# Kernel optimization log

Hardware: AMD Instinct MI355X
Metric: run time of the kernel (lower is better)

Reference implementation:

```python
import jax, jax.numpy as jnp
import numpy as np

NUM_HEADS = 8
EPS = 1e-3

N_TOKENS = 32768
DIM = 256
N_WIN = 128
WIN = N_TOKENS // N_WIN  # 256 tokens per window


def setup_inputs() -> dict:
    key = jax.random.key(0)
    ks = jax.random.split(key, 4)
    x = jax.random.normal(ks[0], (N_TOKENS, DIM), dtype=jnp.float32)
    # torch nn.Linear weights are [out_features, in_features]
    w_qkv = jax.random.normal(ks[1], (3 * DIM, DIM), dtype=jnp.float32) * (DIM ** -0.5)
    w_proj = jax.random.normal(ks[2], (DIM, DIM), dtype=jnp.float32) * (DIM ** -0.5)
    b_proj = jnp.zeros((DIM,), dtype=jnp.float32)
    batch_win_inds = (jnp.arange(N_TOKENS) // WIN).astype(jnp.int64)
    offsets = (jnp.arange(N_WIN) * WIN).astype(jnp.int64)
    counts = jnp.full((N_WIN,), WIN, dtype=jnp.int64)
    return {"x": x, "w_qkv": w_qkv, "w_proj": w_proj, "b_proj": b_proj,
            "offsets": offsets, "counts": counts, "batch_win_inds": batch_win_inds}


def reference(x, w_qkv, w_proj, b_proj, offsets, counts, batch_win_inds):
    N, C = x.shape
    H = NUM_HEADS
    hd = C // H
    W = counts.shape[0]  # number of windows (static)

    qkv = x @ w_qkv.T                      # [N, 3C]
    q, k, v = jnp.split(qkv, 3, axis=-1)   # each [N, C]
    q = jax.nn.relu(q.reshape(N, H, hd))   # [N, H, hd]
    k = jax.nn.relu(k.reshape(N, H, hd))
    v = v.reshape(N, H, hd)

    seg = batch_win_inds.astype(jnp.int32)
    # per-window KV state: kv[w] = sum_{i in w} k_i^T v_i   -> [W, H, hd, hd]
    kv = jax.ops.segment_sum(jnp.einsum('nhc,nhd->nhcd', k, v), seg, num_segments=W)
    # per-window key sum for normalizer                      -> [W, H, hd]
    s = jax.ops.segment_sum(k, seg, num_segments=W)

    y = jnp.einsum('nhc,nhcd->nhd', q, kv[seg])              # [N, H, hd]
    z = jnp.sum(s[seg] * q, axis=-1, keepdims=True)          # [N, H, 1]
    y = y / (z + EPS)

    y = y.reshape(N, C) @ w_proj.T + b_proj                  # [N, C]
    return y
```

## Files before the change

kernel.cpp:

```cpp
#include <hip/hip_runtime.h>

typedef __bf16 bf16_t;
typedef bf16_t bf16x8 __attribute__((ext_vector_type(8)));
typedef bf16_t bf16x4 __attribute__((ext_vector_type(4)));
typedef float f32x4 __attribute__((ext_vector_type(4)));

#define KDIM 256
#define NWIN 128
#define WIN  256

__device__ __forceinline__ bf16x8 cvt8(f32x4 a, f32x4 b) {
    bf16x8 o;
    o[0] = (bf16_t)a[0]; o[1] = (bf16_t)a[1]; o[2] = (bf16_t)a[2]; o[3] = (bf16_t)a[3];
    o[4] = (bf16_t)b[0]; o[5] = (bf16_t)b[1]; o[6] = (bf16_t)b[2]; o[7] = (bf16_t)b[3];
    return o;
}

template<int A_FP32, int F32OUT>
__global__ __launch_bounds__(256) void gemm_lds(
    const void* __restrict__ A_,
    const float* __restrict__ Bw,
    void* __restrict__ Cout,
    int N,
    const float* __restrict__ bias,
    int relu_cols)
{
    __shared__ __align__(16) bf16_t As[128 * 40];
    __shared__ __align__(16) bf16_t Bs[128 * 40];

    const int tid  = threadIdx.x;
    const int lane = tid & 63;
    const int wv   = tid >> 6;
    const int wm   = wv >> 1;
    const int wn   = wv & 1;
    const int m0   = blockIdx.x * 128;
    const int n0   = blockIdx.y * 128;
    const int r    = lane & 15;
    const int q    = lane >> 4;
    const int srow = tid >> 1;
    const int shalf = tid & 1;

    f32x4 acc[4][4] = {};

#pragma unroll
    for (int kc = 0; kc < KDIM; kc += 32) {
        if (A_FP32) {
            const float* ap = (const float*)A_ + (size_t)(m0 + srow) * KDIM + kc + shalf * 16;
            f32x4 f0 = *(const f32x4*)(ap + 0);
            f32x4 f1 = *(const f32x4*)(ap + 4);
            f32x4 f2 = *(const f32x4*)(ap + 8);
            f32x4 f3 = *(const f32x4*)(ap + 12);
            *(bf16x8*)(&As[srow * 40 + shalf * 16 + 0]) = cvt8(f0, f1);
            *(bf16x8*)(&As[srow * 40 + shalf * 16 + 8]) = cvt8(f2, f3);
        } else {
            const bf16_t* ap = (const bf16_t*)A_ + (size_t)(m0 + srow) * KDIM + kc + shalf * 16;
            bf16x8 h0 = *(const bf16x8*)(ap + 0);
            bf16x8 h1 = *(const bf16x8*)(ap + 8);
            *(bf16x8*)(&As[srow * 40 + shalf * 16 + 0]) = h0;
            *(bf16x8*)(&As[srow * 40 + shalf * 16 + 8]) = h1;
        }
        {
            const float* bp = Bw + (size_t)(n0 + srow) * KDIM + kc + shalf * 16;
            f32x4 f0 = *(const f32x4*)(bp + 0);
            f32x4 f1 = *(const f32x4*)(bp + 4);
            f32x4 f2 = *(const f32x4*)(bp + 8);
            f32x4 f3 = *(const f32x4*)(bp + 12);
            *(bf16x8*)(&Bs[srow * 40 + shalf * 16 + 0]) = cvt8(f0, f1);
            *(bf16x8*)(&Bs[srow * 40 + shalf * 16 + 8]) = cvt8(f2, f3);
        }
        __syncthreads();

        bf16x8 a[4], b[4];
#pragma unroll
        for (int i = 0; i < 4; ++i)
            a[i] = *(const bf16x8*)(&As[(wm * 64 + i * 16 + r) * 40 + q * 8]);
#pragma unroll
        for (int j = 0; j < 4; ++j)
            b[j] = *(const bf16x8*)(&Bs[(wn * 64 + j * 16 + r) * 40 + q * 8]);
#pragma unroll
        for (int i = 0; i < 4; ++i)
#pragma unroll
            for (int j = 0; j < 4; ++j)
                acc[i][j] = __builtin_amdgcn_mfma_f32_16x16x32_bf16(a[i], b[j], acc[i][j], 0, 0, 0);
        __syncthreads();
    }

#pragma unroll
    for (int i = 0; i < 4; ++i) {
#pragma unroll
        for (int j = 0; j < 4; ++j) {
            const int colg = n0 + wn * 64 + j * 16 + r;
            float badd = bias ? bias[colg] : 0.0f;
#pragma unroll
            for (int reg = 0; reg < 4; ++reg) {
                const int rowg = m0 + wm * 64 + i * 16 + q * 4 + reg;
                float v = acc[i][j][reg] + badd;
                if (colg < relu_cols) v = fmaxf(v, 0.0f);
                const size_t idx = (size_t)rowg * N + colg;
                if (F32OUT) ((float*)Cout)[idx] = v;
                else        ((bf16_t*)Cout)[idx] = (bf16_t)v;
            }
        }
    }
}

__global__ __launch_bounds__(256) void kvy_kernel(
    const bf16_t* __restrict__ QKV,
    const int* __restrict__ offsets,
    const int* __restrict__ counts,
    bf16_t* __restrict__ Y)
{
    const int w = blockIdx.x;
    const int h = blockIdx.y;
    const int is64 = (counts[1] == 0) ? 1 : 0;
    const int off = offsets[w << is64];
    const int tid = threadIdx.x;
    const int lane = tid & 63;
    const int wv = tid >> 6;

    __shared__ __align__(16) bf16_t KT[32 * 264];
    __shared__ __align__(16) bf16_t VT[32 * 264];
    __shared__ __align__(16) bf16_t KVT[32 * 40];
    __shared__ float sbuf[32];
    __shared__ float spart[32 * 8];
    __shared__ float zinv[WIN];

    {
        const int t = tid;
        const bf16_t* kp = QKV + (size_t)(off + t) * 768 + 256 + h * 32;
        const bf16_t* vp = kp + 256;
        bf16_t ka[32], va[32];
#pragma unroll
        for (int u = 0; u < 4; ++u) {
            bf16x8 kk = *(const bf16x8*)(kp + u * 8);
            bf16x8 vvv = *(const bf16x8*)(vp + u * 8);
#pragma unroll
            for (int j = 0; j < 8; ++j) { ka[u * 8 + j] = kk[j]; va[u * 8 + j] = vvv[j]; }
        }
#pragma unroll
        for (int c = 0; c < 32; ++c) {
            KT[c * 264 + t] = ka[c];
            VT[c * 264 + t] = va[c];
        }
    }
    __syncthreads();

    {
        const int c = tid >> 3;
        const int tc = (tid & 7) * 32;
        float ps = 0.f;
#pragma unroll
        for (int u = 0; u < 4; ++u) {
            bf16x8 kk = *(const bf16x8*)(&KT[c * 264 + tc + u * 8]);
#pragma unroll
            for (int j = 0; j < 8; ++j) ps += (float)kk[j];
        }
        spart[c * 8 + (tid & 7)] = ps;
    }
    {
        const int i = wv >> 1, j = wv & 1;
        const int r = lane & 15, q = lane >> 4;
        f32x4 acc = {};
#pragma unroll
        for (int ch = 0; ch < 8; ++ch) {
            bf16x8 af = *(const bf16x8*)(&KT[(i * 16 + r) * 264 + ch * 32 + q * 8]);
            bf16x8 bf_ = *(const bf16x8*)(&VT[(j * 16 + r) * 264 + ch * 32 + q * 8]);
            acc = __builtin_amdgcn_mfma_f32_16x16x32_bf16(af, bf_, acc, 0, 0, 0);
        }
        bf16x4 kv4;
#pragma unroll
        for (int reg = 0; reg < 4; ++reg) kv4[reg] = (bf16_t)acc[reg];
        *(bf16x4*)(&KVT[(j * 16 + r) * 40 + i * 16 + q * 4]) = kv4;
    }
    __syncthreads();
    if (tid < 32) {
        float s = 0.f;
#pragma unroll
        for (int u = 0; u < 8; ++u) s += spart[tid * 8 + u];
        sbuf[tid] = s;
    }
    __syncthreads();

    {
        const int t = tid;
        const bf16_t* qp = QKV + (size_t)(off + t) * 768 + h * 32;
        float z = 0.f;
#pragma unroll
        for (int u = 0; u < 4; ++u) {
            bf16x8 qq = *(const bf16x8*)(qp + u * 8);
#pragma unroll
            for (int j = 0; j < 8; ++j) z += (float)qq[j] * sbuf[u * 8 + j];
        }
        zinv[t] = 1.0f / (z + 1e-3f);
    }
    __syncthreads();

    {
        const int r = lane & 15, q = lane >> 4;
        bf16x8 b0 = *(const bf16x8*)(&KVT[(r) * 40 + q * 8]);
        bf16x8 b1 = *(const bf16x8*)(&KVT[(16 + r) * 40 + q * 8]);
#pragma unroll
        for (int u = 0; u < 4; ++u) {
            const int mi = wv * 4 + u;
            const bf16_t* ap = QKV + (size_t)(off + mi * 16 + r) * 768 + h * 32 + q * 8;
            bf16x8 af = *(const bf16x8*)ap;
            f32x4 acc0 = {}, acc1 = {};
            acc0 = __builtin_amdgcn_mfma_f32_16x16x32_bf16(af, b0, acc0, 0, 0, 0);
            acc1 = __builtin_amdgcn_mfma_f32_16x16x32_bf16(af, b1, acc1, 0, 0, 0);
#pragma unroll
            for (int reg = 0; reg < 4; ++reg) {
                const int row = mi * 16 + q * 4 + reg;
                const float zi = zinv[row];
                bf16_t* yp = Y + (size_t)(off + row) * 256 + h * 32;
                yp[r]      = (bf16_t)(acc0[reg] * zi);
                yp[16 + r] = (bf16_t)(acc1[reg] * zi);
            }
        }
    }
}

extern "C" void kernel_launch(void* const* d_in, const int* in_sizes, int n_in,
                              void* d_out, int out_size, void* d_ws, size_t ws_size,
                              hipStream_t stream) {
    const float* x      = (const float*)d_in[0];
    const float* w_qkv  = (const float*)d_in[1];
    const float* w_proj = (const float*)d_in[2];
    const float* b_proj = (const float*)d_in[3];
    const int*   offs   = (const int*)d_in[4];
    const int*   cnts   = (const int*)d_in[5];

    const int NX = in_sizes[0];
    const int M  = NX / KDIM;

    char* ws = (char*)d_ws;
    bf16_t* QKV = (bf16_t*)ws;
    bf16_t* Y   = (bf16_t*)(ws + 50331648);
    float*  out = (float*)d_out;

    gemm_lds<1, 0><<<dim3(M / 128, 768 / 128), 256, 0, stream>>>(
        (const void*)x, w_qkv, (void*)QKV, 768, nullptr, 512);

    kvy_kernel<<<dim3(NWIN, 8), 256, 0, stream>>>(QKV, offs, cnts, Y);

    gemm_lds<0, 1><<<dim3(M / 128, 256 / 128), 256, 0, stream>>>(
        (const void*)Y, w_proj, (void*)out, 256, b_proj, 0);
}
```

Baseline: 156.8 us.

## Stage full K=256 tiles in LDS once and drop per-chunk barriers in GEMMs

The GEMM kernels now load the entire 128x256 A and B tiles into dynamic LDS (about 132 KB) in one up-front phase, then run all eight k-chunks of MFMA with no __syncthreads in the loop. This removes 16 barriers per block and lets the global loads issue back-to-back instead of one small chunk at a time. The cost is a large LDS footprint that allows only one block per CU, and no overlap between loading and compute, since the whole load phase finishes before any MFMA work starts.

```diff
diff --git a/kernel.cpp b/kernel.cpp
--- a/kernel.cpp
+++ b/kernel.cpp
@@ -8,6 +8,8 @@
 #define KDIM 256
 #define NWIN 128
 #define WIN  256
+#define LDS_STRIDE 264
+#define GEMM_LDS_BYTES (2 * 128 * LDS_STRIDE * 2)
 
 __device__ __forceinline__ bf16x8 cvt8(f32x4 a, f32x4 b) {
     bf16x8 o;
@@ -17,7 +19,7 @@
 }
 
 template<int A_FP32, int F32OUT>
-__global__ __launch_bounds__(256) void gemm_lds(
+__global__ __launch_bounds__(256) void gemm_os(
     const void* __restrict__ A_,
     const float* __restrict__ Bw,
     void* __restrict__ Cout,
@@ -25,64 +27,62 @@
     const float* __restrict__ bias,
     int relu_cols)
 {
-    __shared__ __align__(16) bf16_t As[128 * 40];
-    __shared__ __align__(16) bf16_t Bs[128 * 40];
-
-    const int tid  = threadIdx.x;
+    extern __shared__ __align__(16) bf16_t lds[];
+    bf16_t* As = lds;
+    bf16_t* Bs = lds + 128 * LDS_STRIDE;
+
+    const int tid = threadIdx.x;
+    const int m0 = blockIdx.x * 128;
+    const int n0 = blockIdx.y * 128;
+
+    const int srow = tid >> 1;
+    const int sh   = (tid & 1) * 128;
+
+    if (A_FP32) {
+        const float* ap = (const float*)A_ + (size_t)(m0 + srow) * KDIM + sh;
+#pragma unroll
+        for (int u = 0; u < 16; ++u) {
+            f32x4 f0 = *(const f32x4*)(ap + u * 8);
+            f32x4 f1 = *(const f32x4*)(ap + u * 8 + 4);
+            *(bf16x8*)(&As[srow * LDS_STRIDE + sh + u * 8]) = cvt8(f0, f1);
+        }
+    } else {
+        const bf16_t* ap = (const bf16_t*)A_ + (size_t)(m0 + srow) * KDIM + sh;
+#pragma unroll
+        for (int u = 0; u < 16; ++u)
+            *(bf16x8*)(&As[srow * LDS_STRIDE + sh + u * 8]) = *(const bf16x8*)(ap + u * 8);
+    }
+    {
+        const float* bp = Bw + (size_t)(n0 + srow) * KDIM + sh;
+#pragma unroll
+        for (int u = 0; u < 16; ++u) {
+            f32x4 f0 = *(const f32x4*)(bp + u * 8);
+            f32x4 f1 = *(const f32x4*)(bp + u * 8 + 4);
+            *(bf16x8*)(&Bs[srow * LDS_STRIDE + sh + u * 8]) = cvt8(f0, f1);
+        }
+    }
+    __syncthreads();
+
     const int lane = tid & 63;
-    const int wv   = tid >> 6;
-    const int wm   = wv >> 1;
-    const int wn   = wv & 1;
-    const int m0   = blockIdx.x * 128;
-    const int n0   = blockIdx.y * 128;
-    const int r    = lane & 15;
-    const int q    = lane >> 4;
-    const int srow = tid >> 1;
-    const int shalf = tid & 1;
+    const int wv = tid >> 6;
+    const int wm = wv >> 1, wn = wv & 1;
+    const int r = lane & 15, q = lane >> 4;
 
     f32x4 acc[4][4] = {};
-
 #pragma unroll
     for (int kc = 0; kc < KDIM; kc += 32) {
-        if (A_FP32) {
-            const float* ap = (const float*)A_ + (size_t)(m0 + srow) * KDIM + kc + shalf * 16;
-            f32x4 f0 = *(const f32x4*)(ap + 0);
-            f32x4 f1 = *(const f32x4*)(ap + 4);
-            f32x4 f2 = *(const f32x4*)(ap + 8);
-            f32x4 f3 = *(const f32x4*)(ap + 12);
-            *(bf16x8*)(&As[srow * 40 + shalf * 16 + 0]) = cvt8(f0, f1);
-            *(bf16x8*)(&As[srow * 40 + shalf * 16 + 8]) = cvt8(f2, f3);
-        } else {
-            const bf16_t* ap = (const bf16_t*)A_ + (size_t)(m0 + srow) * KDIM + kc + shalf * 16;
-            bf16x8 h0 = *(const bf16x8*)(ap + 0);
-            bf16x8 h1 = *(const bf16x8*)(ap + 8);
-            *(bf16x8*)(&As[srow * 40 + shalf * 16 + 0]) = h0;
-            *(bf16x8*)(&As[srow * 40 + shalf * 16 + 8]) = h1;
-        }
-        {
-            const float* bp = Bw + (size_t)(n0 + srow) * KDIM + kc + shalf * 16;
-            f32x4 f0 = *(const f32x4*)(bp + 0);
-            f32x4 f1 = *(const f32x4*)(bp + 4);
-            f32x4 f2 = *(const f32x4*)(bp + 8);
-            f32x4 f3 = *(const f32x4*)(bp + 12);
-            *(bf16x8*)(&Bs[srow * 40 + shalf * 16 + 0]) = cvt8(f0, f1);
-            *(bf16x8*)(&Bs[srow * 40 + shalf * 16 + 8]) = cvt8(f2, f3);
-        }
-        __syncthreads();
-
         bf16x8 a[4], b[4];
 #pragma unroll
         for (int i = 0; i < 4; ++i)
-            a[i] = *(const bf16x8*)(&As[(wm * 64 + i * 16 + r) * 40 + q * 8]);
+            a[i] = *(const bf16x8*)(&As[(wm * 64 + i * 16 + r) * LDS_STRIDE + kc + q * 8]);
 #pragma unroll
         for (int j = 0; j < 4; ++j)
-            b[j] = *(const bf16x8*)(&Bs[(wn * 64 + j * 16 + r) * 40 + q * 8]);
+            b[j] = *(const bf16x8*)(&Bs[(wn * 64 + j * 16 + r) * LDS_STRIDE + kc + q * 8]);
 #pragma unroll
         for (int i = 0; i < 4; ++i)
 #pragma unroll
             for (int j = 0; j < 4; ++j)
                 acc[i][j] = __builtin_amdgcn_mfma_f32_16x16x32_bf16(a[i], b[j], acc[i][j], 0, 0, 0);
-        __syncthreads();
     }
 
 #pragma unroll
@@ -237,11 +237,20 @@
     bf16_t* Y   = (bf16_t*)(ws + 50331648);
     float*  out = (float*)d_out;
 
-    gemm_lds<1, 0><<<dim3(M / 128, 768 / 128), 256, 0, stream>>>(
+    static bool attr_done = false;
+    if (!attr_done) {
+        hipFuncSetAttribute((const void*)gemm_os<1, 0>,
+                            hipFuncAttributeMaxDynamicSharedMemorySize, GEMM_LDS_BYTES);
+        hipFuncSetAttribute((const void*)gemm_os<0, 1>,
+                            hipFuncAttributeMaxDynamicSharedMemorySize, GEMM_LDS_BYTES);
+        attr_done = true;
+    }
+
+    gemm_os<1, 0><<<dim3(M / 128, 768 / 128), 256, GEMM_LDS_BYTES, stream>>>(
         (const void*)x, w_qkv, (void*)QKV, 768, nullptr, 512);
 
     kvy_kernel<<<dim3(NWIN, 8), 256, 0, stream>>>(QKV, offs, cnts, Y);
 
-    gemm_lds<0, 1><<<dim3(M / 128, 256 / 128), 256, 0, stream>>>(
+    gemm_os<0, 1><<<dim3(M / 128, 256 / 128), 256, GEMM_LDS_BYTES, stream>>>(
         (const void*)Y, w_proj, (void*)out, 256, b_proj, 0);
 }
```

Result: slower. 212.3 us (+35.4%).
